# Kernel tuning notes

Hardware: AMD Instinct MI355X
Metric: run time of the kernel (lower is better)

Reference implementation:

```python
import jax, jax.numpy as jnp
import numpy as np

ATT_DIM = 512
HEADS = 8
HEAD_DIM = ATT_DIM // HEADS
D_IN = 512
LEFT_MASK = 256
RIGHT_MASK = 0
LARGE = 1e30


def pos_encoding(S, d):
    # Transformer-XL sinusoid table over relative positions S-1 .. -(S-1), length 2S-1.
    inv_freq = (1.0 / (10000.0 ** (np.arange(0, d, 2.0) / d))).astype(np.float32)
    pos = jnp.arange(S - 1, -S, -1, dtype=jnp.float32)          # [2S-1]
    ang = pos[:, None] * jnp.asarray(inv_freq)[None, :]          # [2S-1, d/2]
    # concat([sin, cos], -1) on a trailing singleton -> interleaved sin/cos per frequency
    return jnp.stack([jnp.sin(ang), jnp.cos(ang)], axis=-1).reshape(2 * S - 1, d)


def rel_shift(x):
    # x: [B, N, S, 2S-1] -> [B, N, S, S] with out[i, j] = x[i, S-1 - i + j]
    B, N, S, L = x.shape
    x = jnp.pad(x, ((0, 0), (0, 0), (0, 0), (1, 0)))             # [B,N,S,L+1]
    x = x.reshape(B, N, L + 1, S)[:, :, 1:, :]                   # [B,N,L,S]
    x = x.reshape(B, N, S, L)
    return x[:, :, :, :S]


def setup_inputs() -> dict:
    key = jax.random.key(0)
    ks = jax.random.split(key, 9)
    B, S, D = 2, 2048, D_IN
    scale = 0.02
    return {
        "x": jax.random.normal(ks[0], (B, S, D), dtype=jnp.float32),
        "Wq": jax.random.normal(ks[1], (D, ATT_DIM), dtype=jnp.float32) * scale,
        "b_con": jax.random.normal(ks[2], (ATT_DIM,), dtype=jnp.float32) * scale,
        "b_rel": jax.random.normal(ks[3], (ATT_DIM,), dtype=jnp.float32) * scale,
        "Wk": jax.random.normal(ks[4], (D, ATT_DIM), dtype=jnp.float32) * scale,
        "Wkr": jax.random.normal(ks[5], (D_IN, ATT_DIM), dtype=jnp.float32) * scale,
        "Wv": jax.random.normal(ks[6], (D, ATT_DIM), dtype=jnp.float32) * scale,
        "bv": jax.random.normal(ks[7], (ATT_DIM,), dtype=jnp.float32) * scale,
        "x_len": jax.random.randint(ks[8], (B,), 1, S + 1).astype(jnp.int32),
    }


def reference(x, Wq, b_con, b_rel, Wk, Wkr, Wv, bv, x_len):
    B, S, D = x.shape
    N, Dh = HEADS, HEAD_DIM

    # content/relative query share the kernel (TiedDense) with separate biases
    q_lin = jnp.einsum('bsd,de->bse', x, Wq)
    q_con = (q_lin + b_con).reshape(B, S, N, Dh)
    q_rel = (q_lin + b_rel).reshape(B, S, N, Dh)
    k_con = jnp.einsum('bsd,de->bse', x, Wk).reshape(B, S, N, Dh)

    content_energy = jnp.einsum('bind,bjnd->bnij', q_con, k_con)  # [B,N,S,S]

    pos_emb = pos_encoding(S, D_IN)                               # [2S-1, D]
    k_rel = (pos_emb @ Wkr).reshape(2 * S - 1, N, Dh)
    relative_energy = jnp.einsum('bind,jnd->bnij', q_rel, k_rel)  # [B,N,S,2S-1]
    relative_energy = rel_shift(relative_energy)                  # [B,N,S,S]

    energy = (content_energy + relative_energy) / jnp.sqrt(jnp.float32(Dh))

    # sequence mask over keys (broadcast [B,1,1,S]) * banded mask (band_part)
    j = jnp.arange(S)
    seq_mask = (j[None, :] < x_len[:, None]).astype(jnp.float32)[:, None, None, :]
    i = jnp.arange(S)[:, None]
    band = ((i - j[None, :] <= LEFT_MASK) & (j[None, :] - i <= RIGHT_MASK)).astype(jnp.float32)
    mask = seq_mask * band[None, None, :, :]

    masked_energy = energy - (1.0 - mask) * LARGE
    attention = jax.nn.softmax(masked_energy, axis=-1)

    v = (jnp.einsum('bsd,de->bse', x, Wv) + bv).reshape(B, S, N, Dh)
    context = jnp.einsum('bnij,bjnd->bind', attention, v).reshape(B, S, N * Dh)
    return context
```

## Files before the change

kernel.cpp:

```cpp
#include <hip/hip_runtime.h>
#include <math.h>

#define S_ 2048
#define NH 8
#define DH 64
#define RSTRIDE 264
#define LP 72

typedef __attribute__((ext_vector_type(8))) short short8;
typedef __attribute__((ext_vector_type(4))) float f32x4;
typedef unsigned short ushort_t;

__device__ __forceinline__ short bf16r(float x) {
    union { float f; unsigned u; } v; v.f = x;
    unsigned r = v.u + 0x7fffu + ((v.u >> 16) & 1u);
    return (short)(r >> 16);
}
__device__ __forceinline__ float b2f(ushort_t h) {
    union { float f; unsigned u; } v; v.u = ((unsigned)h) << 16; return v.f;
}

__global__ __launch_bounds__(256) void prep_kernel(
    const float* __restrict__ Wq, const float* __restrict__ Wk,
    const float* __restrict__ Wv, const float* __restrict__ Wkr,
    ushort_t* __restrict__ WTq, ushort_t* __restrict__ WTk,
    ushort_t* __restrict__ WTv, ushort_t* __restrict__ WTkr,
    ushort_t* __restrict__ pos)
{
    const int widx = blockIdx.z;
    const int t = threadIdx.x;
    if (widx == 4) {
        const int base = blockIdx.y * 8 + blockIdx.x;
        const float C = -0.051905126482615036f;
        const int f = t;
#pragma unroll
        for (int rep = 0; rep < 6; ++rep) {
            const int r = base + rep * 64;
            unsigned pk = 0;
            if (r <= 256) {
                float ang = (float)r * exp2f(C * (float)f);
                unsigned s = (unsigned)(ushort_t)bf16r(sinf(ang));
                unsigned c = (unsigned)(ushort_t)bf16r(cosf(ang));
                pk = s | (c << 16);
            }
            ((unsigned*)pos)[(size_t)r * 256 + f] = pk;
        }
        return;
    }
    const float* W = (widx == 0) ? Wq : (widx == 1) ? Wk : (widx == 2) ? Wv : Wkr;
    ushort_t* WT   = (widx == 0) ? WTq : (widx == 1) ? WTk : (widx == 2) ? WTv : WTkr;
    const int k0 = blockIdx.x * 64, n0 = blockIdx.y * 64;
    __shared__ __align__(16) ushort_t T[64][72];
    const int srow = t >> 2, sc0 = (t & 3) * 16;
    const float* src = &W[(size_t)(k0 + srow) * 512 + n0 + sc0];
#pragma unroll
    for (int u = 0; u < 16; ++u) T[sc0 + u][srow] = (ushort_t)bf16r(src[u]);
    __syncthreads();
    ushort_t* dst = &WT[(size_t)(n0 + srow) * 512 + k0 + sc0];
    *(short8*)dst       = *(const short8*)&T[srow][sc0];
    *(short8*)(dst + 8) = *(const short8*)&T[srow][sc0 + 8];
}

__global__ __launch_bounds__(256) void qkv_gemm(
    const float* __restrict__ x,
    const ushort_t* __restrict__ WTq, const ushort_t* __restrict__ WTk,
    const ushort_t* __restrict__ WTv,
    const ushort_t* __restrict__ pos, const ushort_t* __restrict__ WTkr,
    const float* __restrict__ b_con, const float* __restrict__ b_rel,
    const float* __restrict__ bv,
    ushort_t* __restrict__ qcon, ushort_t* __restrict__ qrel,
    ushort_t* __restrict__ kout, ushort_t* __restrict__ vT,
    ushort_t* __restrict__ krel)
{
    const int widx = blockIdx.y >> 3;
    const int tid = threadIdx.x, lane = tid & 63, w = tid >> 6;
    const int quad = lane >> 4, l16 = lane & 15;

    __shared__ __align__(16) ushort_t A_lds[128][40];
    __shared__ __align__(16) ushort_t B_lds[64][40];

    f32x4 acc[2][4];
#pragma unroll
    for (int mt = 0; mt < 2; ++mt)
#pragma unroll
        for (int nt = 0; nt < 4; ++nt) acc[mt][nt] = (f32x4){0.f, 0.f, 0.f, 0.f};

    const int arow = tid >> 1, ak0 = (tid & 1) * 16;
    const int brow = tid >> 2, bk0 = (tid & 3) * 8;

    if (widx < 2) {
        const int m0 = blockIdx.x * 128;
        const int n0 = (blockIdx.y & 7) * 64;
        const ushort_t* WT = (widx == 0) ? WTq : WTk;

        for (int k0 = 0; k0 < 512; k0 += 32) {
            const float* xs = &x[(size_t)(m0 + arow) * 512 + k0 + ak0];
            ushort_t t16[16];
#pragma unroll
            for (int u = 0; u < 16; ++u) t16[u] = (ushort_t)bf16r(xs[u]);
            *(short8*)&A_lds[arow][ak0]     = *(short8*)&t16[0];
            *(short8*)&A_lds[arow][ak0 + 8] = *(short8*)&t16[8];
            *(short8*)&B_lds[brow][bk0] =
                *(const short8*)&WT[(size_t)(n0 + brow) * 512 + k0 + bk0];
            __syncthreads();
            short8 a0 = *(const short8*)&A_lds[w * 32 + l16][quad * 8];
            short8 a1 = *(const short8*)&A_lds[w * 32 + 16 + l16][quad * 8];
#pragma unroll
            for (int nt = 0; nt < 4; ++nt) {
                short8 bb = *(const short8*)&B_lds[nt * 16 + l16][quad * 8];
                acc[0][nt] = __builtin_amdgcn_mfma_f32_16x16x32_bf16(a0, bb, acc[0][nt], 0, 0, 0);
                acc[1][nt] = __builtin_amdgcn_mfma_f32_16x16x32_bf16(a1, bb, acc[1][nt], 0, 0, 0);
            }
            __syncthreads();
        }

#pragma unroll
        for (int nt = 0; nt < 4; ++nt) {
            const int col = n0 + nt * 16 + l16;
            float bc = 0.f, br = 0.f;
            if (widx == 0) { bc = b_con[col]; br = b_rel[col]; }
#pragma unroll
            for (int mt = 0; mt < 2; ++mt) {
#pragma unroll
                for (int reg = 0; reg < 4; ++reg) {
                    const size_t m = (size_t)(m0 + w * 32 + mt * 16 + quad * 4 + reg);
                    const float val = acc[mt][nt][reg];
                    if (widx == 0) {
                        qcon[m * 512 + col] = (ushort_t)bf16r((val + bc) * 0.125f);
                        qrel[m * 512 + col] = (ushort_t)bf16r((val + br) * 0.125f);
                    } else {
                        kout[m * 512 + col] = (ushort_t)bf16r(val);
                    }
                }
            }
        }
    } else if (widx == 2) {
        const int vb = (blockIdx.y & 7) * 32 + blockIdx.x;
        const int m0d = (vb & 3) * 128;
        const int n0j = (vb >> 2) * 64;

        for (int k0 = 0; k0 < 512; k0 += 32) {
            *(short8*)&A_lds[arow][ak0] =
                *(const short8*)&WTv[(size_t)(m0d + arow) * 512 + k0 + ak0];
            *(short8*)&A_lds[arow][ak0 + 8] =
                *(const short8*)&WTv[(size_t)(m0d + arow) * 512 + k0 + ak0 + 8];
            const float* xs = &x[(size_t)(n0j + brow) * 512 + k0 + bk0];
            ushort_t t8[8];
#pragma unroll
            for (int u = 0; u < 8; ++u) t8[u] = (ushort_t)bf16r(xs[u]);
            *(short8*)&B_lds[brow][bk0] = *(short8*)&t8[0];
            __syncthreads();
            short8 a0 = *(const short8*)&A_lds[w * 32 + l16][quad * 8];
            short8 a1 = *(const short8*)&A_lds[w * 32 + 16 + l16][quad * 8];
#pragma unroll
            for (int nt = 0; nt < 4; ++nt) {
                short8 bb = *(const short8*)&B_lds[nt * 16 + l16][quad * 8];
                acc[0][nt] = __builtin_amdgcn_mfma_f32_16x16x32_bf16(a0, bb, acc[0][nt], 0, 0, 0);
                acc[1][nt] = __builtin_amdgcn_mfma_f32_16x16x32_bf16(a1, bb, acc[1][nt], 0, 0, 0);
            }
            __syncthreads();
        }

        const int b = n0j >> 11;
#pragma unroll
        for (int mt = 0; mt < 2; ++mt) {
#pragma unroll
            for (int reg = 0; reg < 4; ++reg) {
                const int d = m0d + w * 32 + mt * 16 + quad * 4 + reg;
                const int n = d >> 6, dd = d & 63;
                const float bvv = bv[d];
#pragma unroll
                for (int nt = 0; nt < 4; ++nt) {
                    const int s = (n0j + nt * 16 + l16) & 2047;
                    vT[((size_t)((b * NH + n) * 64 + dd)) * 2048 + s] =
                        (ushort_t)bf16r(acc[mt][nt][reg] + bvv);
                }
            }
        }
    } else {
        if (blockIdx.x >= 24) return;
        const int m0 = (blockIdx.x >> 3) * 128;
        const int n0 = (blockIdx.x & 7) * 64;

        for (int k0 = 0; k0 < 512; k0 += 32) {
            const ushort_t* ps = &pos[(size_t)(m0 + arow) * 512 + k0 + ak0];
            *(short8*)&A_lds[arow][ak0]     = *(const short8*)ps;
            *(short8*)&A_lds[arow][ak0 + 8] = *(const short8*)(ps + 8);
            *(short8*)&B_lds[brow][bk0] =
                *(const short8*)&WTkr[(size_t)(n0 + brow) * 512 + k0 + bk0];
            __syncthreads();
            short8 a0 = *(const short8*)&A_lds[w * 32 + l16][quad * 8];
            short8 a1 = *(const short8*)&A_lds[w * 32 + 16 + l16][quad * 8];
#pragma unroll
            for (int nt = 0; nt < 4; ++nt) {
                short8 bb = *(const short8*)&B_lds[nt * 16 + l16][quad * 8];
                acc[0][nt] = __builtin_amdgcn_mfma_f32_16x16x32_bf16(a0, bb, acc[0][nt], 0, 0, 0);
                acc[1][nt] = __builtin_amdgcn_mfma_f32_16x16x32_bf16(a1, bb, acc[1][nt], 0, 0, 0);
            }
            __syncthreads();
        }

#pragma unroll
        for (int nt = 0; nt < 4; ++nt) {
            const int col = n0 + nt * 16 + l16;
#pragma unroll
            for (int mt = 0; mt < 2; ++mt)
#pragma unroll
                for (int reg = 0; reg < 4; ++reg) {
                    const size_t m = (size_t)(m0 + w * 32 + mt * 16 + quad * 4 + reg);
                    krel[m * 512 + col] = (ushort_t)bf16r(acc[mt][nt][reg]);
                }
        }
    }
}

__global__ __launch_bounds__(256) void rel_gemm(
    const ushort_t* __restrict__ qrel, const ushort_t* __restrict__ krel,
    const ushort_t* __restrict__ vT, ushort_t* __restrict__ R,
    float* __restrict__ vmean)
{
    const int tile = blockIdx.x, n = blockIdx.y, b = blockIdx.z;
    const int tid = threadIdx.x, lane = tid & 63, w = tid >> 6;
    const int quad = lane >> 4, l16 = lane & 15;

    __shared__ __align__(16) ushort_t A_lds[128][LP];
    __shared__ __align__(16) ushort_t B_lds[64][LP];

    if (tile == 16) {
        const int row = tid >> 2, seg = tid & 3;
        const ushort_t* src = &vT[((size_t)((b * NH + n) * 64 + row)) * 2048 + seg * 512];
        float sum = 0.f;
        for (int it = 0; it < 64; ++it) {
            short8 h = *(const short8*)(src + it * 8);
#pragma unroll
            for (int u = 0; u < 8; ++u) sum += b2f((ushort_t)h[u]);
        }
        float* scratch = (float*)A_lds;
        scratch[row * 4 + seg] = sum;
        __syncthreads();
        if (tid < 64) {
            float s = scratch[tid * 4] + scratch[tid * 4 + 1]
                    + scratch[tid * 4 + 2] + scratch[tid * 4 + 3];
            vmean[(size_t)b * 512 + n * 64 + tid] = s * (1.0f / (float)S_);
        }
        return;
    }

    const int i0 = tile * 128;
    {
        const int srow = tid >> 1, sc0 = (tid & 1) * 32;
        const ushort_t* src = &qrel[((size_t)b * S_ + i0 + srow) * 512 + n * 64 + sc0];
#pragma unroll
        for (int u = 0; u < 4; ++u)
            *(short8*)&A_lds[srow][sc0 + u * 8] = *(const short8*)(src + u * 8);
    }

    const size_t rbase = ((size_t)(b * NH + n) * S_ + i0) * RSTRIDE;
    const int srow2 = tid >> 2, sc2 = (tid & 3) * 16;

#pragma unroll 1
    for (int rc = 0; rc < 5; ++rc) {
        __syncthreads();
        {
            const ushort_t* src = &krel[(size_t)(rc * 64 + srow2) * 512 + n * 64 + sc2];
            *(short8*)&B_lds[srow2][sc2]     = *(const short8*)src;
            *(short8*)&B_lds[srow2][sc2 + 8] = *(const short8*)(src + 8);
        }
        __syncthreads();

        short8 a[2][2];
#pragma unroll
        for (int mt = 0; mt < 2; ++mt) {
            a[mt][0] = *(const short8*)&A_lds[w * 32 + mt * 16 + l16][quad * 8];
            a[mt][1] = *(const short8*)&A_lds[w * 32 + mt * 16 + l16][quad * 8 + 32];
        }
#pragma unroll
        for (int nt = 0; nt < 4; ++nt) {
            short8 b0 = *(const short8*)&B_lds[nt * 16 + l16][quad * 8];
            short8 b1 = *(const short8*)&B_lds[nt * 16 + l16][quad * 8 + 32];
            const int r = rc * 64 + nt * 16 + l16;
#pragma unroll
            for (int mt = 0; mt < 2; ++mt) {
                f32x4 s = (f32x4){0.f, 0.f, 0.f, 0.f};
                s = __builtin_amdgcn_mfma_f32_16x16x32_bf16(a[mt][0], b0, s, 0, 0, 0);
                s = __builtin_amdgcn_mfma_f32_16x16x32_bf16(a[mt][1], b1, s, 0, 0, 0);
                if (r < RSTRIDE) {
#pragma unroll
                    for (int reg = 0; reg < 4; ++reg) {
                        const int i = w * 32 + mt * 16 + quad * 4 + reg;
                        R[rbase + (size_t)i * RSTRIDE + r] = (ushort_t)bf16r(s[reg]);
                    }
                }
            }
        }
    }
}

__global__ __launch_bounds__(128) void attn_kernel(
    const ushort_t* __restrict__ qcon, const ushort_t* __restrict__ kbuf,
    const ushort_t* __restrict__ vT, const ushort_t* __restrict__ R,
    const float* __restrict__ vmean, const int* __restrict__ xlen_p,
    float* __restrict__ out)
{
    const int bx = blockIdx.x;
    const int tile = ((bx & 7) << 3) | (bx >> 3);
    const int n = blockIdx.y, b = blockIdx.z;
    const int i0 = tile * 32;
    const int tid = threadIdx.x, lane = tid & 63, w = tid >> 6;
    const int quad = lane >> 4, l16 = lane & 15;
    const int xlen = xlen_p[b];

    __shared__ __align__(16) ushort_t q_lds[32][LP];
    __shared__ __align__(16) ushort_t k_lds[64][LP];
    __shared__ __align__(16) ushort_t vT_lds[64][LP];
    __shared__ __align__(16) ushort_t p_lds[32][LP];

    {
        const int qr = tid >> 2, qc = (tid & 3) * 16;
        const ushort_t* src = &qcon[((size_t)b * S_ + i0 + qr) * 512 + n * 64 + qc];
        *(short8*)&q_lds[qr][qc]     = *(const short8*)src;
        *(short8*)&q_lds[qr][qc + 8] = *(const short8*)(src + 8);
    }

    f32x4 Oa[4];
#pragma unroll
    for (int nt = 0; nt < 4; ++nt) Oa[nt] = (f32x4){0.f, 0.f, 0.f, 0.f};
    float lpart[4] = {};

    const size_t rrowB = (size_t)(b * NH + n) * S_ * RSTRIDE;
    const size_t vTbase = (size_t)((b * NH + n) * 64) * 2048;
    const int srow = tid >> 1, sc0 = (tid & 1) * 32;
    const short8 z8 = {0, 0, 0, 0, 0, 0, 0, 0};

    short8 kr[4], vr[4], kn[4], vn[4];
    ushort_t rc_[16], rn_[16];

    auto issue = [&](int c, short8* kd, short8* vd, ushort_t* rd) {
        const int jc0 = i0 - 256 + c * 64;
        const int jg = jc0 + srow;
        const bool okk = (jg >= 0);
        const ushort_t* ks = &kbuf[((size_t)b * S_ + jg) * 512 + n * 64 + sc0];
        const ushort_t* vs = &vT[vTbase + (size_t)srow * 2048 + jc0 + sc0];
#pragma unroll
        for (int u = 0; u < 4; ++u) {
            kd[u] = okk ? *(const short8*)(ks + u * 8) : z8;
            const bool okv = (jc0 + sc0 + u * 8) >= 0;
            vd[u] = okv ? *(const short8*)(vs + u * 8) : z8;
        }
#pragma unroll
        for (int jt = 0; jt < 4; ++jt) {
#pragma unroll
            for (int reg = 0; reg < 4; ++reg) {
                const int i = i0 + w * 16 + quad * 4 + reg;
                const int j = jc0 + jt * 16 + l16;
                const int r = i - j;
                const bool valid = (j >= 0) && (j < xlen) && (r >= 0) && (r <= 256);
                rd[jt * 4 + reg] = valid ? R[rrowB + (size_t)i * RSTRIDE + r]
                                         : (ushort_t)0;
            }
        }
    };

    issue(0, kr, vr, rc_);

#pragma unroll 1
    for (int c = 0; c < 5; ++c) {
        const int jc0 = i0 - 256 + c * 64;
        __syncthreads();
#pragma unroll
        for (int u = 0; u < 4; ++u) {
            *(short8*)&k_lds[srow][sc0 + u * 8]  = kr[u];
            *(short8*)&vT_lds[srow][sc0 + u * 8] = vr[u];
        }
        if (c < 4) issue(c + 1, kn, vn, rn_);
        __syncthreads();

        short8 aq0 = *(const short8*)&q_lds[w * 16 + l16][quad * 8];
        short8 aq1 = *(const short8*)&q_lds[w * 16 + l16][quad * 8 + 32];
        f32x4 Sacc[4];
#pragma unroll
        for (int jt = 0; jt < 4; ++jt) {
            short8 bk0 = *(const short8*)&k_lds[jt * 16 + l16][quad * 8];
            short8 bk1 = *(const short8*)&k_lds[jt * 16 + l16][quad * 8 + 32];
            f32x4 s = (f32x4){0.f, 0.f, 0.f, 0.f};
            s = __builtin_amdgcn_mfma_f32_16x16x32_bf16(aq0, bk0, s, 0, 0, 0);
            s = __builtin_amdgcn_mfma_f32_16x16x32_bf16(aq1, bk1, s, 0, 0, 0);
            Sacc[jt] = s;
        }

#pragma unroll
        for (int jt = 0; jt < 4; ++jt) {
#pragma unroll
            for (int reg = 0; reg < 4; ++reg) {
                const int i = i0 + w * 16 + quad * 4 + reg;
                const int j = jc0 + jt * 16 + l16;
                const int r = i - j;
                const bool valid = (j >= 0) && (j < xlen) && (r >= 0) && (r <= 256);
                float e = valid ? __expf(Sacc[jt][reg] + b2f(rc_[jt * 4 + reg])) : 0.f;
                lpart[reg] += e;
                p_lds[w * 16 + quad * 4 + reg][jt * 16 + l16] = (ushort_t)bf16r(e);
            }
        }
        __syncthreads();

        short8 ap0 = *(const short8*)&p_lds[w * 16 + l16][quad * 8];
        short8 ap1 = *(const short8*)&p_lds[w * 16 + l16][quad * 8 + 32];
#pragma unroll
        for (int nt = 0; nt < 4; ++nt) {
            short8 bv0 = *(const short8*)&vT_lds[nt * 16 + l16][quad * 8];
            short8 bv1 = *(const short8*)&vT_lds[nt * 16 + l16][quad * 8 + 32];
            Oa[nt] = __builtin_amdgcn_mfma_f32_16x16x32_bf16(ap0, bv0, Oa[nt], 0, 0, 0);
            Oa[nt] = __builtin_amdgcn_mfma_f32_16x16x32_bf16(ap1, bv1, Oa[nt], 0, 0, 0);
        }

#pragma unroll
        for (int u = 0; u < 4; ++u) { kr[u] = kn[u]; vr[u] = vn[u]; }
#pragma unroll
        for (int u = 0; u < 16; ++u) rc_[u] = rn_[u];
    }

#pragma unroll
    for (int reg = 0; reg < 4; ++reg) {
#pragma unroll
        for (int off = 1; off < 16; off <<= 1)
            lpart[reg] += __shfl_xor(lpart[reg], off, 64);
    }

#pragma unroll
    for (int reg = 0; reg < 4; ++reg) {
        const int i = i0 + w * 16 + quad * 4 + reg;
        const bool dead = (i >= xlen + 256);
        const float linv = 1.0f / lpart[reg];
#pragma unroll
        for (int nt = 0; nt < 4; ++nt) {
            const int d = n * 64 + nt * 16 + l16;
            float val = dead ? vmean[(size_t)b * 512 + d] : Oa[nt][reg] * linv;
            out[((size_t)b * S_ + i) * 512 + d] = val;
        }
    }
}

extern "C" void kernel_launch(void* const* d_in, const int* in_sizes, int n_in,
                              void* d_out, int out_size, void* d_ws, size_t ws_size,
                              hipStream_t stream) {
    const float* x     = (const float*)d_in[0];
    const float* Wq    = (const float*)d_in[1];
    const float* b_con = (const float*)d_in[2];
    const float* b_rel = (const float*)d_in[3];
    const float* Wk    = (const float*)d_in[4];
    const float* Wkr   = (const float*)d_in[5];
    const float* Wv    = (const float*)d_in[6];
    const float* bv    = (const float*)d_in[7];
    const int*   xlen  = (const int*)d_in[8];
    float* out = (float*)d_out;

    float* ws = (float*)d_ws;
    float* vmean = ws;
    ushort_t* ub   = (ushort_t*)(vmean + 1024);
    ushort_t* R    = ub;
    ushort_t* qcon = R    + 8650752;
    ushort_t* kbuf = qcon + 2097152;
    ushort_t* vT   = kbuf + 2097152;
    ushort_t* qrel = vT   + 2097152;
    ushort_t* krel = qrel + 2097152;
    ushort_t* pos  = krel + 196608;
    ushort_t* WTq  = pos  + 196608;
    ushort_t* WTk  = WTq + 262144;
    ushort_t* WTv  = WTk + 262144;
    ushort_t* WTkr = WTv + 262144;

    prep_kernel<<<dim3(8, 8, 5), 256, 0, stream>>>(Wq, Wk, Wv, Wkr,
                                                   WTq, WTk, WTv, WTkr, pos);
    qkv_gemm<<<dim3(32, 25), 256, 0, stream>>>(x, WTq, WTk, WTv, pos, WTkr,
                                               b_con, b_rel, bv,
                                               qcon, qrel, kbuf, vT, krel);
    rel_gemm<<<dim3(17, 8, 2), 256, 0, stream>>>(qrel, krel, vT, R, vmean);
    attn_kernel<<<dim3(64, 8, 2), 128, 0, stream>>>(qcon, kbuf, vT, R, vmean,
                                                    xlen, out);
}
```

Baseline: 146.6 us.

## Fuse prep, projection and relative GEMM into one cooperative persistent kernel

Merges the weight-transpose/pos-encoding prep, the QKV/krel projection GEMM and the relative-score GEMM into one cooperative kernel of 512 blocks separated by grid-wide syncs, with fallback to three separate launches if the cooperative launch fails. The projection GEMM is re-tiled to 64x64 tiles processed in a persistent task loop, with register prefetch of the next K slice. The relative GEMM also prefetches krel into registers. This is meant to remove launch gaps and tail effects between the small front-end kernels. In exchange it adds grid-sync cost, uses smaller tiles with less reuse, and depends on all 512 blocks being co-resident.

```diff
diff --git a/kernel.cpp b/kernel.cpp
--- a/kernel.cpp
+++ b/kernel.cpp
@@ -1,11 +1,14 @@
 #include <hip/hip_runtime.h>
+#include <hip/hip_cooperative_groups.h>
 #include <math.h>
 
 #define S_ 2048
 #define NH 8
-#define DH 64
 #define RSTRIDE 264
 #define LP 72
+#define ARENA_SHORTS 13824
+
+namespace cg = cooperative_groups;
 
 typedef __attribute__((ext_vector_type(8))) short short8;
 typedef __attribute__((ext_vector_type(4))) float f32x4;
@@ -20,19 +23,34 @@
     union { float f; unsigned u; } v; v.u = ((unsigned)h) << 16; return v.f;
 }
 
-__global__ __launch_bounds__(256) void prep_kernel(
+
+__device__ __forceinline__ void phaseA(
+    int bid, int tid, ushort_t* arena,
     const float* __restrict__ Wq, const float* __restrict__ Wk,
     const float* __restrict__ Wv, const float* __restrict__ Wkr,
     ushort_t* __restrict__ WTq, ushort_t* __restrict__ WTk,
     ushort_t* __restrict__ WTv, ushort_t* __restrict__ WTkr,
     ushort_t* __restrict__ pos)
 {
-    const int widx = blockIdx.z;
-    const int t = threadIdx.x;
-    if (widx == 4) {
-        const int base = blockIdx.y * 8 + blockIdx.x;
+    if (bid < 256) {
+        const int widx = bid >> 6;
+        const float* W = (widx == 0) ? Wq : (widx == 1) ? Wk : (widx == 2) ? Wv : Wkr;
+        ushort_t* WT   = (widx == 0) ? WTq : (widx == 1) ? WTk : (widx == 2) ? WTv : WTkr;
+        const int sub = bid & 63;
+        const int k0 = (sub >> 3) * 64, n0 = (sub & 7) * 64;
+        ushort_t (*T)[72] = (ushort_t(*)[72])arena;
+        const int srow = tid >> 2, sc0 = (tid & 3) * 16;
+        const float* src = &W[(size_t)(k0 + srow) * 512 + n0 + sc0];
+#pragma unroll
+        for (int u = 0; u < 16; ++u) T[sc0 + u][srow] = (ushort_t)bf16r(src[u]);
+        __syncthreads();
+        ushort_t* dst = &WT[(size_t)(n0 + srow) * 512 + k0 + sc0];
+        *(short8*)dst       = *(const short8*)&T[srow][sc0];
+        *(short8*)(dst + 8) = *(const short8*)&T[srow][sc0 + 8];
+    } else if (bid < 320) {
+        const int base = bid - 256;
         const float C = -0.051905126482615036f;
-        const int f = t;
+        const int f = tid;
 #pragma unroll
         for (int rep = 0; rep < 6; ++rep) {
             const int r = base + rep * 64;
@@ -45,23 +63,11 @@
             }
             ((unsigned*)pos)[(size_t)r * 256 + f] = pk;
         }
-        return;
-    }
-    const float* W = (widx == 0) ? Wq : (widx == 1) ? Wk : (widx == 2) ? Wv : Wkr;
-    ushort_t* WT   = (widx == 0) ? WTq : (widx == 1) ? WTk : (widx == 2) ? WTv : WTkr;
-    const int k0 = blockIdx.x * 64, n0 = blockIdx.y * 64;
-    __shared__ __align__(16) ushort_t T[64][72];
-    const int srow = t >> 2, sc0 = (t & 3) * 16;
-    const float* src = &W[(size_t)(k0 + srow) * 512 + n0 + sc0];
-#pragma unroll
-    for (int u = 0; u < 16; ++u) T[sc0 + u][srow] = (ushort_t)bf16r(src[u]);
-    __syncthreads();
-    ushort_t* dst = &WT[(size_t)(n0 + srow) * 512 + k0 + sc0];
-    *(short8*)dst       = *(const short8*)&T[srow][sc0];
-    *(short8*)(dst + 8) = *(const short8*)&T[srow][sc0 + 8];
-}
-
-__global__ __launch_bounds__(256) void qkv_gemm(
+    }
+}
+
+__device__ __forceinline__ void phaseB(
+    int bid, int tid, ushort_t* arena,
     const float* __restrict__ x,
     const ushort_t* __restrict__ WTq, const ushort_t* __restrict__ WTk,
     const ushort_t* __restrict__ WTv,
@@ -69,173 +75,182 @@
     const float* __restrict__ b_con, const float* __restrict__ b_rel,
     const float* __restrict__ bv,
     ushort_t* __restrict__ qcon, ushort_t* __restrict__ qrel,
-    ushort_t* __restrict__ kout, ushort_t* __restrict__ vT,
+    ushort_t* __restrict__ kbuf, ushort_t* __restrict__ vT,
     ushort_t* __restrict__ krel)
 {
-    const int widx = blockIdx.y >> 3;
-    const int tid = threadIdx.x, lane = tid & 63, w = tid >> 6;
+    const int lane = tid & 63, w4 = tid >> 6;
     const int quad = lane >> 4, l16 = lane & 15;
-
-    __shared__ __align__(16) ushort_t A_lds[128][40];
-    __shared__ __align__(16) ushort_t B_lds[64][40];
-
-    f32x4 acc[2][4];
-#pragma unroll
-    for (int mt = 0; mt < 2; ++mt)
-#pragma unroll
-        for (int nt = 0; nt < 4; ++nt) acc[mt][nt] = (f32x4){0.f, 0.f, 0.f, 0.f};
-
-    const int arow = tid >> 1, ak0 = (tid & 1) * 16;
-    const int brow = tid >> 2, bk0 = (tid & 3) * 8;
-
-    if (widx < 2) {
-        const int m0 = blockIdx.x * 128;
-        const int n0 = (blockIdx.y & 7) * 64;
-        const ushort_t* WT = (widx == 0) ? WTq : WTk;
-
-        for (int k0 = 0; k0 < 512; k0 += 32) {
-            const float* xs = &x[(size_t)(m0 + arow) * 512 + k0 + ak0];
-            ushort_t t16[16];
-#pragma unroll
-            for (int u = 0; u < 16; ++u) t16[u] = (ushort_t)bf16r(xs[u]);
-            *(short8*)&A_lds[arow][ak0]     = *(short8*)&t16[0];
-            *(short8*)&A_lds[arow][ak0 + 8] = *(short8*)&t16[8];
-            *(short8*)&B_lds[brow][bk0] =
-                *(const short8*)&WT[(size_t)(n0 + brow) * 512 + k0 + bk0];
-            __syncthreads();
-            short8 a0 = *(const short8*)&A_lds[w * 32 + l16][quad * 8];
-            short8 a1 = *(const short8*)&A_lds[w * 32 + 16 + l16][quad * 8];
+    ushort_t (*A_lds)[40] = (ushort_t(*)[40])arena;
+    ushort_t (*B_lds)[40] = (ushort_t(*)[40])(arena + 2560);
+    const int arow = tid >> 2, ak0 = (tid & 3) * 8;
+
+    for (int task = bid; task < 1584; task += 512) {
+        f32x4 acc[4];
+#pragma unroll
+        for (int nt = 0; nt < 4; ++nt) acc[nt] = (f32x4){0.f, 0.f, 0.f, 0.f};
+
+        if (task < 1024) {
+            const int widx = task >> 9;
+            const int rem = task & 511;
+            const int m0 = (rem >> 3) * 64, n0 = (rem & 7) * 64;
+            const ushort_t* WT = (widx == 0) ? WTq : WTk;
+            const float* xrow = &x[(size_t)(m0 + arow) * 512 + ak0];
+            const ushort_t* wrow = &WT[(size_t)(n0 + arow) * 512 + ak0];
+            float4 pa0 = *(const float4*)xrow;
+            float4 pa1 = *(const float4*)(xrow + 4);
+            short8 pb = *(const short8*)wrow;
+#pragma unroll 1
+            for (int k0 = 0; k0 < 512; k0 += 32) {
+                __syncthreads();
+                {
+                    float pf[8];
+                    *(float4*)&pf[0] = pa0; *(float4*)&pf[4] = pa1;
+                    ushort_t t8[8];
+#pragma unroll
+                    for (int u = 0; u < 8; ++u) t8[u] = (ushort_t)bf16r(pf[u]);
+                    *(short8*)&A_lds[arow][ak0] = *(short8*)&t8[0];
+                    *(short8*)&B_lds[arow][ak0] = pb;
+                }
+                if (k0 < 480) {
+                    pa0 = *(const float4*)(xrow + k0 + 32);
+                    pa1 = *(const float4*)(xrow + k0 + 36);
+                    pb  = *(const short8*)(wrow + k0 + 32);
+                }
+                __syncthreads();
+                short8 a0 = *(const short8*)&A_lds[w4 * 16 + l16][quad * 8];
+#pragma unroll
+                for (int nt = 0; nt < 4; ++nt) {
+                    short8 bb = *(const short8*)&B_lds[nt * 16 + l16][quad * 8];
+                    acc[nt] = __builtin_amdgcn_mfma_f32_16x16x32_bf16(a0, bb, acc[nt], 0, 0, 0);
+                }
+            }
 #pragma unroll
             for (int nt = 0; nt < 4; ++nt) {
-                short8 bb = *(const short8*)&B_lds[nt * 16 + l16][quad * 8];
-                acc[0][nt] = __builtin_amdgcn_mfma_f32_16x16x32_bf16(a0, bb, acc[0][nt], 0, 0, 0);
-                acc[1][nt] = __builtin_amdgcn_mfma_f32_16x16x32_bf16(a1, bb, acc[1][nt], 0, 0, 0);
-            }
-            __syncthreads();
-        }
-
-#pragma unroll
-        for (int nt = 0; nt < 4; ++nt) {
-            const int col = n0 + nt * 16 + l16;
-            float bc = 0.f, br = 0.f;
-            if (widx == 0) { bc = b_con[col]; br = b_rel[col]; }
-#pragma unroll
-            for (int mt = 0; mt < 2; ++mt) {
+                const int col = n0 + nt * 16 + l16;
+                float bc = 0.f, br = 0.f;
+                if (widx == 0) { bc = b_con[col]; br = b_rel[col]; }
 #pragma unroll
                 for (int reg = 0; reg < 4; ++reg) {
-                    const size_t m = (size_t)(m0 + w * 32 + mt * 16 + quad * 4 + reg);
-                    const float val = acc[mt][nt][reg];
+                    const size_t m = (size_t)(m0 + w4 * 16 + quad * 4 + reg);
+                    const float val = acc[nt][reg];
                     if (widx == 0) {
                         qcon[m * 512 + col] = (ushort_t)bf16r((val + bc) * 0.125f);
                         qrel[m * 512 + col] = (ushort_t)bf16r((val + br) * 0.125f);
                     } else {
-                        kout[m * 512 + col] = (ushort_t)bf16r(val);
+                        kbuf[m * 512 + col] = (ushort_t)bf16r(val);
                     }
                 }
             }
-        }
-    } else if (widx == 2) {
-        const int vb = (blockIdx.y & 7) * 32 + blockIdx.x;
-        const int m0d = (vb & 3) * 128;
-        const int n0j = (vb >> 2) * 64;
-
-        for (int k0 = 0; k0 < 512; k0 += 32) {
-            *(short8*)&A_lds[arow][ak0] =
-                *(const short8*)&WTv[(size_t)(m0d + arow) * 512 + k0 + ak0];
-            *(short8*)&A_lds[arow][ak0 + 8] =
-                *(const short8*)&WTv[(size_t)(m0d + arow) * 512 + k0 + ak0 + 8];
-            const float* xs = &x[(size_t)(n0j + brow) * 512 + k0 + bk0];
-            ushort_t t8[8];
-#pragma unroll
-            for (int u = 0; u < 8; ++u) t8[u] = (ushort_t)bf16r(xs[u]);
-            *(short8*)&B_lds[brow][bk0] = *(short8*)&t8[0];
-            __syncthreads();
-            short8 a0 = *(const short8*)&A_lds[w * 32 + l16][quad * 8];
-            short8 a1 = *(const short8*)&A_lds[w * 32 + 16 + l16][quad * 8];
+        } else if (task < 1536) {
+            const int vt = task - 1024;
+            const int m0d = (vt & 7) * 64;
+            const int n0j = (vt >> 3) * 64;
+            const ushort_t* wrow = &WTv[(size_t)(m0d + arow) * 512 + ak0];
+            const float* xrow = &x[(size_t)(n0j + arow) * 512 + ak0];
+            short8 pa = *(const short8*)wrow;
+            float4 pb0 = *(const float4*)xrow;
+            float4 pb1 = *(const float4*)(xrow + 4);
+#pragma unroll 1
+            for (int k0 = 0; k0 < 512; k0 += 32) {
+                __syncthreads();
+                {
+                    *(short8*)&A_lds[arow][ak0] = pa;
+                    float pf[8];
+                    *(float4*)&pf[0] = pb0; *(float4*)&pf[4] = pb1;
+                    ushort_t t8[8];
+#pragma unroll
+                    for (int u = 0; u < 8; ++u) t8[u] = (ushort_t)bf16r(pf[u]);
+                    *(short8*)&B_lds[arow][ak0] = *(short8*)&t8[0];
+                }
+                if (k0 < 480) {
+                    pa  = *(const short8*)(wrow + k0 + 32);
+                    pb0 = *(const float4*)(xrow + k0 + 32);
+                    pb1 = *(const float4*)(xrow + k0 + 36);
+                }
+                __syncthreads();
+                short8 a0 = *(const short8*)&A_lds[w4 * 16 + l16][quad * 8];
+#pragma unroll
+                for (int nt = 0; nt < 4; ++nt) {
+                    short8 bb = *(const short8*)&B_lds[nt * 16 + l16][quad * 8];
+                    acc[nt] = __builtin_amdgcn_mfma_f32_16x16x32_bf16(a0, bb, acc[nt], 0, 0, 0);
+                }
+            }
+            float bvv[4];
+#pragma unroll
+            for (int reg = 0; reg < 4; ++reg)
+                bvv[reg] = bv[m0d + w4 * 16 + quad * 4 + reg];
 #pragma unroll
             for (int nt = 0; nt < 4; ++nt) {
-                short8 bb = *(const short8*)&B_lds[nt * 16 + l16][quad * 8];
-                acc[0][nt] = __builtin_amdgcn_mfma_f32_16x16x32_bf16(a0, bb, acc[0][nt], 0, 0, 0);
-                acc[1][nt] = __builtin_amdgcn_mfma_f32_16x16x32_bf16(a1, bb, acc[1][nt], 0, 0, 0);
-            }
-            __syncthreads();
-        }
-
-        const int b = n0j >> 11;
-#pragma unroll
-        for (int mt = 0; mt < 2; ++mt) {
-#pragma unroll
-            for (int reg = 0; reg < 4; ++reg) {
-                const int d = m0d + w * 32 + mt * 16 + quad * 4 + reg;
-                const int n = d >> 6, dd = d & 63;
-                const float bvv = bv[d];
+                const int sg = n0j + nt * 16 + l16;
+                const int b = sg >> 11, s = sg & 2047;
+#pragma unroll
+                for (int reg = 0; reg < 4; ++reg) {
+                    const int d = m0d + w4 * 16 + quad * 4 + reg;
+                    const int n = d >> 6, dd = d & 63;
+                    vT[((size_t)((b * NH + n) * 64 + dd)) * 2048 + s] =
+                        (ushort_t)bf16r(acc[nt][reg] + bvv[reg]);
+                }
+            }
+        } else {
+            const int kt = task - 1536;
+            const int m0 = (kt >> 3) * 64, n0 = (kt & 7) * 64;
+            const ushort_t* prow = &pos[(size_t)(m0 + arow) * 512 + ak0];
+            const ushort_t* wrow = &WTkr[(size_t)(n0 + arow) * 512 + ak0];
+            short8 pa = *(const short8*)prow;
+            short8 pb = *(const short8*)wrow;
+#pragma unroll 1
+            for (int k0 = 0; k0 < 512; k0 += 32) {
+                __syncthreads();
+                *(short8*)&A_lds[arow][ak0] = pa;
+                *(short8*)&B_lds[arow][ak0] = pb;
+                if (k0 < 480) {
+                    pa = *(const short8*)(prow + k0 + 32);
+                    pb = *(const short8*)(wrow + k0 + 32);
+                }
+                __syncthreads();
+                short8 a0 = *(const short8*)&A_lds[w4 * 16 + l16][quad * 8];
 #pragma unroll
                 for (int nt = 0; nt < 4; ++nt) {
-                    const int s = (n0j + nt * 16 + l16) & 2047;
-                    vT[((size_t)((b * NH + n) * 64 + dd)) * 2048 + s] =
-                        (ushort_t)bf16r(acc[mt][nt][reg] + bvv);
-                }
-            }
-        }
-    } else {
-        if (blockIdx.x >= 24) return;
-        const int m0 = (blockIdx.x >> 3) * 128;
-        const int n0 = (blockIdx.x & 7) * 64;
-
-        for (int k0 = 0; k0 < 512; k0 += 32) {
-            const ushort_t* ps = &pos[(size_t)(m0 + arow) * 512 + k0 + ak0];
-            *(short8*)&A_lds[arow][ak0]     = *(const short8*)ps;
-            *(short8*)&A_lds[arow][ak0 + 8] = *(const short8*)(ps + 8);
-            *(short8*)&B_lds[brow][bk0] =
-                *(const short8*)&WTkr[(size_t)(n0 + brow) * 512 + k0 + bk0];
-            __syncthreads();
-            short8 a0 = *(const short8*)&A_lds[w * 32 + l16][quad * 8];
-            short8 a1 = *(const short8*)&A_lds[w * 32 + 16 + l16][quad * 8];
+                    short8 bb = *(const short8*)&B_lds[nt * 16 + l16][quad * 8];
+                    acc[nt] = __builtin_amdgcn_mfma_f32_16x16x32_bf16(a0, bb, acc[nt], 0, 0, 0);
+                }
+            }
 #pragma unroll
             for (int nt = 0; nt < 4; ++nt) {
-                short8 bb = *(const short8*)&B_lds[nt * 16 + l16][quad * 8];
-                acc[0][nt] = __builtin_amdgcn_mfma_f32_16x16x32_bf16(a0, bb, acc[0][nt], 0, 0, 0);
-                acc[1][nt] = __builtin_amdgcn_mfma_f32_16x16x32_bf16(a1, bb, acc[1][nt], 0, 0, 0);
-            }
-            __syncthreads();
-        }
-
-#pragma unroll
-        for (int nt = 0; nt < 4; ++nt) {
-            const int col = n0 + nt * 16 + l16;
-#pragma unroll
-            for (int mt = 0; mt < 2; ++mt)
+                const int col = n0 + nt * 16 + l16;
 #pragma unroll
                 for (int reg = 0; reg < 4; ++reg) {
-                    const size_t m = (size_t)(m0 + w * 32 + mt * 16 + quad * 4 + reg);
-                    krel[m * 512 + col] = (ushort_t)bf16r(acc[mt][nt][reg]);
-                }
-        }
-    }
-}
-
-__global__ __launch_bounds__(256) void rel_gemm(
+                    const size_t m = (size_t)(m0 + w4 * 16 + quad * 4 + reg);
+                    krel[m * 512 + col] = (ushort_t)bf16r(acc[nt][reg]);
+                }
+            }
+        }
+    }
+}
+
+__device__ __forceinline__ void phaseC(
+    int bid, int tid, ushort_t* arena,
     const ushort_t* __restrict__ qrel, const ushort_t* __restrict__ krel,
     const ushort_t* __restrict__ vT, ushort_t* __restrict__ R,
     float* __restrict__ vmean)
 {
-    const int tile = blockIdx.x, n = blockIdx.y, b = blockIdx.z;
-    const int tid = threadIdx.x, lane = tid & 63, w = tid >> 6;
+    const int lane = tid & 63, w4 = tid >> 6;
     const int quad = lane >> 4, l16 = lane & 15;
 
-    __shared__ __align__(16) ushort_t A_lds[128][LP];
-    __shared__ __align__(16) ushort_t B_lds[64][LP];
-
-    if (tile == 16) {
+    if (bid >= 272) return;
+    if (bid >= 256) {
+        const int vt = bid - 256;
+        const int b = vt >> 3, n = vt & 7;
         const int row = tid >> 2, seg = tid & 3;
-        const ushort_t* src = &vT[((size_t)((b * NH + n) * 64 + row)) * 2048 + seg * 512];
+        const ushort_t* src =
+            &vT[((size_t)((b * NH + n) * 64 + row)) * 2048 + seg * 512];
         float sum = 0.f;
         for (int it = 0; it < 64; ++it) {
             short8 h = *(const short8*)(src + it * 8);
 #pragma unroll
             for (int u = 0; u < 8; ++u) sum += b2f((ushort_t)h[u]);
         }
-        float* scratch = (float*)A_lds;
+        float* scratch = (float*)arena;
         scratch[row * 4 + seg] = sum;
         __syncthreads();
         if (tid < 64) {
@@ -246,38 +261,44 @@
         return;
     }
 
+    const int tile = bid & 15, n = (bid >> 4) & 7, b = bid >> 7;
     const int i0 = tile * 128;
+    ushort_t (*A2)[LP] = (ushort_t(*)[LP])arena;
+    ushort_t (*B2)[LP] = (ushort_t(*)[LP])(arena + 9216);
     {
-        const int srow = tid >> 1, sc0 = (tid & 1) * 32;
-        const ushort_t* src = &qrel[((size_t)b * S_ + i0 + srow) * 512 + n * 64 + sc0];
+        const int srow = tid >> 1, sc0b = (tid & 1) * 32;
+        const ushort_t* src = &qrel[((size_t)b * S_ + i0 + srow) * 512 + n * 64 + sc0b];
 #pragma unroll
         for (int u = 0; u < 4; ++u)
-            *(short8*)&A_lds[srow][sc0 + u * 8] = *(const short8*)(src + u * 8);
-    }
-
+            *(short8*)&A2[srow][sc0b + u * 8] = *(const short8*)(src + u * 8);
+    }
     const size_t rbase = ((size_t)(b * NH + n) * S_ + i0) * RSTRIDE;
     const int srow2 = tid >> 2, sc2 = (tid & 3) * 16;
-
+    const ushort_t* kr0 = &krel[(size_t)srow2 * 512 + n * 64 + sc2];
+    short8 pb0 = *(const short8*)kr0;
+    short8 pb1 = *(const short8*)(kr0 + 8);
 #pragma unroll 1
     for (int rc = 0; rc < 5; ++rc) {
         __syncthreads();
-        {
-            const ushort_t* src = &krel[(size_t)(rc * 64 + srow2) * 512 + n * 64 + sc2];
-            *(short8*)&B_lds[srow2][sc2]     = *(const short8*)src;
-            *(short8*)&B_lds[srow2][sc2 + 8] = *(const short8*)(src + 8);
-        }
-        __syncthreads();
-
+        *(short8*)&B2[srow2][sc2]     = pb0;
+        *(short8*)&B2[srow2][sc2 + 8] = pb1;
+        if (rc < 4) {
+            const ushort_t* src =
+                &krel[(size_t)((rc + 1) * 64 + srow2) * 512 + n * 64 + sc2];
+            pb0 = *(const short8*)src;
+            pb1 = *(const short8*)(src + 8);
+        }
+        __syncthreads();
         short8 a[2][2];
 #pragma unroll
         for (int mt = 0; mt < 2; ++mt) {
-            a[mt][0] = *(const short8*)&A_lds[w * 32 + mt * 16 + l16][quad * 8];
-            a[mt][1] = *(const short8*)&A_lds[w * 32 + mt * 16 + l16][quad * 8 + 32];
+            a[mt][0] = *(const short8*)&A2[w4 * 32 + mt * 16 + l16][quad * 8];
+            a[mt][1] = *(const short8*)&A2[w4 * 32 + mt * 16 + l16][quad * 8 + 32];
         }
 #pragma unroll
         for (int nt = 0; nt < 4; ++nt) {
-            short8 b0 = *(const short8*)&B_lds[nt * 16 + l16][quad * 8];
-            short8 b1 = *(const short8*)&B_lds[nt * 16 + l16][quad * 8 + 32];
+            short8 b0 = *(const short8*)&B2[nt * 16 + l16][quad * 8];
+            short8 b1 = *(const short8*)&B2[nt * 16 + l16][quad * 8 + 32];
             const int r = rc * 64 + nt * 16 + l16;
 #pragma unroll
             for (int mt = 0; mt < 2; ++mt) {
@@ -287,13 +308,65 @@
                 if (r < RSTRIDE) {
 #pragma unroll
                     for (int reg = 0; reg < 4; ++reg) {
-                        const int i = w * 32 + mt * 16 + quad * 4 + reg;
+                        const int i = w4 * 32 + mt * 16 + quad * 4 + reg;
                         R[rbase + (size_t)i * RSTRIDE + r] = (ushort_t)bf16r(s[reg]);
                     }
                 }
             }
         }
     }
+}
+
+__global__ __launch_bounds__(256, 2) void fused_front(
+    const float* __restrict__ x,
+    const float* __restrict__ Wq, const float* __restrict__ Wk,
+    const float* __restrict__ Wv, const float* __restrict__ Wkr,
+    const float* __restrict__ b_con, const float* __restrict__ b_rel,
+    const float* __restrict__ bv,
+    ushort_t* __restrict__ WTq, ushort_t* __restrict__ WTk,
+    ushort_t* __restrict__ WTv, ushort_t* __restrict__ WTkr,
+    ushort_t* __restrict__ pos,
+    ushort_t* __restrict__ qcon, ushort_t* __restrict__ qrel,
+    ushort_t* __restrict__ kbuf, ushort_t* __restrict__ vT,
+    ushort_t* __restrict__ krel, ushort_t* __restrict__ R,
+    float* __restrict__ vmean)
+{
+    cg::grid_group grid = cg::this_grid();
+    __shared__ __align__(16) ushort_t arena[ARENA_SHORTS];
+    phaseA(blockIdx.x, threadIdx.x, arena, Wq, Wk, Wv, Wkr,
+           WTq, WTk, WTv, WTkr, pos);
+    __threadfence();
+    grid.sync();
+    phaseB(blockIdx.x, threadIdx.x, arena, x, WTq, WTk, WTv, pos, WTkr,
+           b_con, b_rel, bv, qcon, qrel, kbuf, vT, krel);
+    __threadfence();
+    grid.sync();
+    phaseC(blockIdx.x, threadIdx.x, arena, qrel, krel, vT, R, vmean);
+}
+
+__global__ __launch_bounds__(256) void kA(
+    const float* Wq, const float* Wk, const float* Wv, const float* Wkr,
+    ushort_t* WTq, ushort_t* WTk, ushort_t* WTv, ushort_t* WTkr, ushort_t* pos)
+{
+    __shared__ __align__(16) ushort_t arena[ARENA_SHORTS];
+    phaseA(blockIdx.x, threadIdx.x, arena, Wq, Wk, Wv, Wkr, WTq, WTk, WTv, WTkr, pos);
+}
+__global__ __launch_bounds__(256) void kB(
+    const float* x, const ushort_t* WTq, const ushort_t* WTk, const ushort_t* WTv,
+    const ushort_t* pos, const ushort_t* WTkr,
+    const float* b_con, const float* b_rel, const float* bv,
+    ushort_t* qcon, ushort_t* qrel, ushort_t* kbuf, ushort_t* vT, ushort_t* krel)
+{
+    __shared__ __align__(16) ushort_t arena[ARENA_SHORTS];
+    phaseB(blockIdx.x, threadIdx.x, arena, x, WTq, WTk, WTv, pos, WTkr,
+           b_con, b_rel, bv, qcon, qrel, kbuf, vT, krel);
+}
+__global__ __launch_bounds__(256) void kC(
+    const ushort_t* qrel, const ushort_t* krel, const ushort_t* vT,
+    ushort_t* R, float* vmean)
+{
+    __shared__ __align__(16) ushort_t arena[ARENA_SHORTS];
+    phaseC(blockIdx.x, threadIdx.x, arena, qrel, krel, vT, R, vmean);
 }
 
 __global__ __launch_bounds__(128) void attn_kernel(
@@ -469,12 +542,24 @@
     ushort_t* WTv  = WTk + 262144;
     ushort_t* WTkr = WTv + 262144;
 
-    prep_kernel<<<dim3(8, 8, 5), 256, 0, stream>>>(Wq, Wk, Wv, Wkr,
-                                                   WTq, WTk, WTv, WTkr, pos);
-    qkv_gemm<<<dim3(32, 25), 256, 0, stream>>>(x, WTq, WTk, WTv, pos, WTkr,
-                                               b_con, b_rel, bv,
-                                               qcon, qrel, kbuf, vT, krel);
-    rel_gemm<<<dim3(17, 8, 2), 256, 0, stream>>>(qrel, krel, vT, R, vmean);
+    void* kargs[] = {
+        (void*)&x, (void*)&Wq, (void*)&Wk, (void*)&Wv, (void*)&Wkr,
+        (void*)&b_con, (void*)&b_rel, (void*)&bv,
+        (void*)&WTq, (void*)&WTk, (void*)&WTv, (void*)&WTkr, (void*)&pos,
+        (void*)&qcon, (void*)&qrel, (void*)&kbuf, (void*)&vT, (void*)&krel,
+        (void*)&R, (void*)&vmean
+    };
+    hipError_t err = hipLaunchCooperativeKernel(
+        (const void*)fused_front, dim3(512), dim3(256), kargs, 0, stream);
+    if (err != hipSuccess) {
+        (void)hipGetLastError();
+        kA<<<dim3(512), 256, 0, stream>>>(Wq, Wk, Wv, Wkr,
+                                          WTq, WTk, WTv, WTkr, pos);
+        kB<<<dim3(512), 256, 0, stream>>>(x, WTq, WTk, WTv, pos, WTkr,
+                                          b_con, b_rel, bv,
+                                          qcon, qrel, kbuf, vT, krel);
+        kC<<<dim3(512), 256, 0, stream>>>(qrel, krel, vT, R, vmean);
+    }
     attn_kernel<<<dim3(64, 8, 2), 128, 0, stream>>>(qcon, kbuf, vT, R, vmean,
                                                     xlen, out);
 }
```

After: 398.2 us. +171.7%, slower.

## Pre-convert x to bf16 and register-prefetch next K tile in GEMMs

Applied to the files above, without the earlier changes.

Adds a sixth slice to the prep kernel that converts x from fp32 to bf16 once. The QKV GEMM then reads 16-byte bf16 vectors instead of converting fp32 on every tile in every block, which was repeated across the eight N-blocks. The QKV and rel GEMM loops now load the next K tile into registers before the MFMA on the current one, overlapping global loads with compute. This costs an extra 4 MB workspace write and read plus one more prep pass.

```diff
diff --git a/kernel.cpp b/kernel.cpp
--- a/kernel.cpp
+++ b/kernel.cpp
@@ -21,11 +21,12 @@
 }
 
 __global__ __launch_bounds__(256) void prep_kernel(
+    const float* __restrict__ x,
     const float* __restrict__ Wq, const float* __restrict__ Wk,
     const float* __restrict__ Wv, const float* __restrict__ Wkr,
     ushort_t* __restrict__ WTq, ushort_t* __restrict__ WTk,
     ushort_t* __restrict__ WTv, ushort_t* __restrict__ WTkr,
-    ushort_t* __restrict__ pos)
+    ushort_t* __restrict__ pos, ushort_t* __restrict__ xb16)
 {
     const int widx = blockIdx.z;
     const int t = threadIdx.x;
@@ -47,6 +48,21 @@
         }
         return;
     }
+    if (widx == 5) {
+        const int sub = blockIdx.y * 8 + blockIdx.x;
+        const size_t base = (size_t)sub * 32768;
+#pragma unroll
+        for (int it = 0; it < 8; ++it) {
+            const size_t idx = base + (size_t)it * 4096 + (size_t)t * 16;
+            const float* src = &x[idx];
+            ushort_t t16[16];
+#pragma unroll
+            for (int u = 0; u < 16; ++u) t16[u] = (ushort_t)bf16r(src[u]);
+            *(short8*)&xb16[idx]     = *(short8*)&t16[0];
+            *(short8*)&xb16[idx + 8] = *(short8*)&t16[8];
+        }
+        return;
+    }
     const float* W = (widx == 0) ? Wq : (widx == 1) ? Wk : (widx == 2) ? Wv : Wkr;
     ushort_t* WT   = (widx == 0) ? WTq : (widx == 1) ? WTk : (widx == 2) ? WTv : WTkr;
     const int k0 = blockIdx.x * 64, n0 = blockIdx.y * 64;
@@ -62,7 +78,7 @@
 }
 
 __global__ __launch_bounds__(256) void qkv_gemm(
-    const float* __restrict__ x,
+    const ushort_t* __restrict__ xb16,
     const ushort_t* __restrict__ WTq, const ushort_t* __restrict__ WTk,
     const ushort_t* __restrict__ WTv,
     const ushort_t* __restrict__ pos, const ushort_t* __restrict__ WTkr,
@@ -92,16 +108,24 @@
         const int m0 = blockIdx.x * 128;
         const int n0 = (blockIdx.y & 7) * 64;
         const ushort_t* WT = (widx == 0) ? WTq : WTk;
-
+        const ushort_t* xrow = &xb16[(size_t)(m0 + arow) * 512 + ak0];
+        const ushort_t* wrow = &WT[(size_t)(n0 + brow) * 512 + bk0];
+
+        short8 pa0 = *(const short8*)xrow;
+        short8 pa1 = *(const short8*)(xrow + 8);
+        short8 pb  = *(const short8*)wrow;
+
+#pragma unroll 1
         for (int k0 = 0; k0 < 512; k0 += 32) {
-            const float* xs = &x[(size_t)(m0 + arow) * 512 + k0 + ak0];
-            ushort_t t16[16];
-#pragma unroll
-            for (int u = 0; u < 16; ++u) t16[u] = (ushort_t)bf16r(xs[u]);
-            *(short8*)&A_lds[arow][ak0]     = *(short8*)&t16[0];
-            *(short8*)&A_lds[arow][ak0 + 8] = *(short8*)&t16[8];
-            *(short8*)&B_lds[brow][bk0] =
-                *(const short8*)&WT[(size_t)(n0 + brow) * 512 + k0 + bk0];
+            __syncthreads();
+            *(short8*)&A_lds[arow][ak0]     = pa0;
+            *(short8*)&A_lds[arow][ak0 + 8] = pa1;
+            *(short8*)&B_lds[brow][bk0]     = pb;
+            if (k0 < 480) {
+                pa0 = *(const short8*)(xrow + k0 + 32);
+                pa1 = *(const short8*)(xrow + k0 + 40);
+                pb  = *(const short8*)(wrow + k0 + 32);
+            }
             __syncthreads();
             short8 a0 = *(const short8*)&A_lds[w * 32 + l16][quad * 8];
             short8 a1 = *(const short8*)&A_lds[w * 32 + 16 + l16][quad * 8];
@@ -111,7 +135,6 @@
                 acc[0][nt] = __builtin_amdgcn_mfma_f32_16x16x32_bf16(a0, bb, acc[0][nt], 0, 0, 0);
                 acc[1][nt] = __builtin_amdgcn_mfma_f32_16x16x32_bf16(a1, bb, acc[1][nt], 0, 0, 0);
             }
-            __syncthreads();
         }
 
 #pragma unroll
@@ -138,17 +161,24 @@
         const int vb = (blockIdx.y & 7) * 32 + blockIdx.x;
         const int m0d = (vb & 3) * 128;
         const int n0j = (vb >> 2) * 64;
-
+        const ushort_t* wrow = &WTv[(size_t)(m0d + arow) * 512 + ak0];
+        const ushort_t* xrow = &xb16[(size_t)(n0j + brow) * 512 + bk0];
+
+        short8 pa0 = *(const short8*)wrow;
+        short8 pa1 = *(const short8*)(wrow + 8);
+        short8 pb  = *(const short8*)xrow;
+
+#pragma unroll 1
         for (int k0 = 0; k0 < 512; k0 += 32) {
-            *(short8*)&A_lds[arow][ak0] =
-                *(const short8*)&WTv[(size_t)(m0d + arow) * 512 + k0 + ak0];
-            *(short8*)&A_lds[arow][ak0 + 8] =
-                *(const short8*)&WTv[(size_t)(m0d + arow) * 512 + k0 + ak0 + 8];
-            const float* xs = &x[(size_t)(n0j + brow) * 512 + k0 + bk0];
-            ushort_t t8[8];
-#pragma unroll
-            for (int u = 0; u < 8; ++u) t8[u] = (ushort_t)bf16r(xs[u]);
-            *(short8*)&B_lds[brow][bk0] = *(short8*)&t8[0];
+            __syncthreads();
+            *(short8*)&A_lds[arow][ak0]     = pa0;
+            *(short8*)&A_lds[arow][ak0 + 8] = pa1;
+            *(short8*)&B_lds[brow][bk0]     = pb;
+            if (k0 < 480) {
+                pa0 = *(const short8*)(wrow + k0 + 32);
+                pa1 = *(const short8*)(wrow + k0 + 40);
+                pb  = *(const short8*)(xrow + k0 + 32);
+            }
             __syncthreads();
             short8 a0 = *(const short8*)&A_lds[w * 32 + l16][quad * 8];
             short8 a1 = *(const short8*)&A_lds[w * 32 + 16 + l16][quad * 8];
@@ -158,7 +188,6 @@
                 acc[0][nt] = __builtin_amdgcn_mfma_f32_16x16x32_bf16(a0, bb, acc[0][nt], 0, 0, 0);
                 acc[1][nt] = __builtin_amdgcn_mfma_f32_16x16x32_bf16(a1, bb, acc[1][nt], 0, 0, 0);
             }
-            __syncthreads();
         }
 
         const int b = n0j >> 11;
@@ -181,13 +210,24 @@
         if (blockIdx.x >= 24) return;
         const int m0 = (blockIdx.x >> 3) * 128;
         const int n0 = (blockIdx.x & 7) * 64;
-
+        const ushort_t* prow = &pos[(size_t)(m0 + arow) * 512 + ak0];
+        const ushort_t* wrow = &WTkr[(size_t)(n0 + brow) * 512 + bk0];
+
+        short8 pa0 = *(const short8*)prow;
+        short8 pa1 = *(const short8*)(prow + 8);
+        short8 pb  = *(const short8*)wrow;
+
+#pragma unroll 1
         for (int k0 = 0; k0 < 512; k0 += 32) {
-            const ushort_t* ps = &pos[(size_t)(m0 + arow) * 512 + k0 + ak0];
-            *(short8*)&A_lds[arow][ak0]     = *(const short8*)ps;
-            *(short8*)&A_lds[arow][ak0 + 8] = *(const short8*)(ps + 8);
-            *(short8*)&B_lds[brow][bk0] =
-                *(const short8*)&WTkr[(size_t)(n0 + brow) * 512 + k0 + bk0];
+            __syncthreads();
+            *(short8*)&A_lds[arow][ak0]     = pa0;
+            *(short8*)&A_lds[arow][ak0 + 8] = pa1;
+            *(short8*)&B_lds[brow][bk0]     = pb;
+            if (k0 < 480) {
+                pa0 = *(const short8*)(prow + k0 + 32);
+                pa1 = *(const short8*)(prow + k0 + 40);
+                pb  = *(const short8*)(wrow + k0 + 32);
+            }
             __syncthreads();
             short8 a0 = *(const short8*)&A_lds[w * 32 + l16][quad * 8];
             short8 a1 = *(const short8*)&A_lds[w * 32 + 16 + l16][quad * 8];
@@ -197,7 +237,6 @@
                 acc[0][nt] = __builtin_amdgcn_mfma_f32_16x16x32_bf16(a0, bb, acc[0][nt], 0, 0, 0);
                 acc[1][nt] = __builtin_amdgcn_mfma_f32_16x16x32_bf16(a1, bb, acc[1][nt], 0, 0, 0);
             }
-            __syncthreads();
         }
 
 #pragma unroll
@@ -258,14 +297,20 @@
     const size_t rbase = ((size_t)(b * NH + n) * S_ + i0) * RSTRIDE;
     const int srow2 = tid >> 2, sc2 = (tid & 3) * 16;
 
+    short8 pb0, pb1;
+    auto issueB = [&](int rc) {
+        const ushort_t* src = &krel[(size_t)(rc * 64 + srow2) * 512 + n * 64 + sc2];
+        pb0 = *(const short8*)src;
+        pb1 = *(const short8*)(src + 8);
+    };
+    issueB(0);
+
 #pragma unroll 1
     for (int rc = 0; rc < 5; ++rc) {
         __syncthreads();
-        {
-            const ushort_t* src = &krel[(size_t)(rc * 64 + srow2) * 512 + n * 64 + sc2];
-            *(short8*)&B_lds[srow2][sc2]     = *(const short8*)src;
-            *(short8*)&B_lds[srow2][sc2 + 8] = *(const short8*)(src + 8);
-        }
+        *(short8*)&B_lds[srow2][sc2]     = pb0;
+        *(short8*)&B_lds[srow2][sc2 + 8] = pb1;
+        if (rc < 4) issueB(rc + 1);
         __syncthreads();
 
         short8 a[2][2];
@@ -462,16 +507,17 @@
     ushort_t* kbuf = qcon + 2097152;
     ushort_t* vT   = kbuf + 2097152;
     ushort_t* qrel = vT   + 2097152;
-    ushort_t* krel = qrel + 2097152;
+    ushort_t* xb16 = qrel + 2097152;
+    ushort_t* krel = xb16 + 2097152;
     ushort_t* pos  = krel + 196608;
     ushort_t* WTq  = pos  + 196608;
     ushort_t* WTk  = WTq + 262144;
     ushort_t* WTv  = WTk + 262144;
     ushort_t* WTkr = WTv + 262144;
 
-    prep_kernel<<<dim3(8, 8, 5), 256, 0, stream>>>(Wq, Wk, Wv, Wkr,
-                                                   WTq, WTk, WTv, WTkr, pos);
-    qkv_gemm<<<dim3(32, 25), 256, 0, stream>>>(x, WTq, WTk, WTv, pos, WTkr,
+    prep_kernel<<<dim3(8, 8, 6), 256, 0, stream>>>(x, Wq, Wk, Wv, Wkr,
+                                                   WTq, WTk, WTv, WTkr, pos, xb16);
+    qkv_gemm<<<dim3(32, 25), 256, 0, stream>>>(xb16, WTq, WTk, WTv, pos, WTkr,
                                                b_con, b_rel, bv,
                                                qcon, qrel, kbuf, vT, krel);
     rel_gemm<<<dim3(17, 8, 2), 256, 0, stream>>>(qrel, krel, vT, R, vmean);
```

Result: no change. 146.6 us (+0.0%).
